# Kernel optimization log

Measured on AMD Instinct MI355X. Metric: run time of the kernel, lower is better.

Reference implementation:

```python
import jax, jax.numpy as jnp
import numpy as np

H = 16
DH = 64
THETA = 10000.0


def setup_inputs() -> dict:
    key = jax.random.key(0)
    ks = jax.random.split(key, 9)
    B, M, R = 4, 1024, 256
    d = H * DH
    s = 0.05
    return {
        "Pq": jax.random.normal(ks[0], (B, M, R), jnp.float32) * s,
        "Pk": jax.random.normal(ks[1], (B, M, R), jnp.float32) * s,
        "Pv": jax.random.normal(ks[2], (B, M, R), jnp.float32) * s,
        "Vq": jax.random.normal(ks[3], (R, d), jnp.float32) * s,
        "Vk": jax.random.normal(ks[4], (R, d), jnp.float32) * s,
        "Vv": jax.random.normal(ks[5], (R, d), jnp.float32) * s,
        "bq": jax.random.normal(ks[6], (d,), jnp.float32) * s,
        "bk": jax.random.normal(ks[7], (d,), jnp.float32) * s,
        "bv": jax.random.normal(ks[8], (d,), jnp.float32) * s,
        "attention_mask": jnp.ones((B, M), jnp.int32),
        "position_ids": jnp.tile(jnp.arange(M, dtype=jnp.int32), (B, 1)),
    }


def _rope_cos_sin(position_ids):
    # half-dim frequencies, matching the kernel's half-half rotation
    half = DH // 2
    inv_freq = 1.0 / (THETA ** (jnp.arange(0, half, dtype=jnp.float32) / half))
    ang = position_ids.astype(jnp.float32)[..., None] * inv_freq  # [B,M,half]
    return jnp.cos(ang), jnp.sin(ang)


def _rotate(x, cos, sin):
    # x: [B,H,M,dh]; cos/sin: [B,M,half] -> broadcast over heads
    half = DH // 2
    x0, x1 = x[..., :half], x[..., half:]
    c = cos[:, None, :, :]
    s = sin[:, None, :, :]
    return jnp.concatenate([x0 * c - x1 * s, x0 * s + x1 * c], axis=-1)


def reference(Pq, Pk, Pv, Vq, Vk, Vv, bq, bk, bv, attention_mask, position_ids):
    B, M, R = Pq.shape
    # reconstruct per-head Q/K/V from low-rank factors
    Vq3 = Vq.reshape(R, H, DH)
    Vk3 = Vk.reshape(R, H, DH)
    Vv3 = Vv.reshape(R, H, DH)
    q = jnp.einsum("bmr,rhd->bhmd", Pq, Vq3) + bq.reshape(H, DH)[None, :, None, :]
    k = jnp.einsum("bmr,rhd->bhmd", Pk, Vk3) + bk.reshape(H, DH)[None, :, None, :]
    v = jnp.einsum("bmr,rhd->bhmd", Pv, Vv3) + bv.reshape(H, DH)[None, :, None, :]
    cos, sin = _rope_cos_sin(position_ids)
    q = _rotate(q, cos, sin)
    k = _rotate(k, cos, sin)
    scale = 1.0 / jnp.sqrt(jnp.float32(DH))
    scores = jnp.einsum("bhmd,bhnd->bhmn", q, k) * scale  # [B,H,M,M]
    valid = attention_mask.astype(bool)
    pad = valid[:, None, :, None] & valid[:, None, None, :]
    scores = jnp.where(pad, scores, -jnp.inf)
    p = jax.nn.softmax(scores, axis=-1)
    out = jnp.einsum("bhmn,bhnd->bhmd", p, v)
    return out
```

## Files before the change

### kernel.cpp

```cpp
#include <hip/hip_runtime.h>
#include <hip/hip_bf16.h>
#include <math.h>

#define BB 4
#define MM 1024
#define RR 256
#define HH 16
#define DHH 64
#define DD (HH*DHH)

typedef __attribute__((ext_vector_type(8))) short short8;
typedef __attribute__((ext_vector_type(4))) float f32x4;

static __device__ __forceinline__ unsigned short f2bf(float x) {
    __hip_bfloat16 h = __float2bfloat16(x);
    return *(unsigned short*)&h;
}

#if defined(__has_builtin)
#  if __has_builtin(__builtin_amdgcn_exp2f)
#    define EXP2F(x) __builtin_amdgcn_exp2f(x)
#  endif
#endif
#ifndef EXP2F
#  define EXP2F(x) __expf((x) * 0.6931471805599453f)
#endif

static __device__ __forceinline__ unsigned pack_bf16_rh(float a, float b) {
    unsigned ua = __builtin_bit_cast(unsigned, a) + 0x8000u;
    unsigned ub = __builtin_bit_cast(unsigned, b) + 0x8000u;
    return __builtin_amdgcn_perm(ub, ua, 0x07060302u);
}

__global__ __launch_bounds__(256) void prep_kernel(
    const float* __restrict__ Pq, const float* __restrict__ Pk, const float* __restrict__ Pv,
    const float* __restrict__ Vq, const float* __restrict__ Vk, const float* __restrict__ Vv,
    __hip_bfloat16* __restrict__ VTq, __hip_bfloat16* __restrict__ VTk,
    __hip_bfloat16* __restrict__ VTv, __hip_bfloat16* __restrict__ Pb)
{
    const int t = threadIdx.x;
    if (blockIdx.x < 768) {
        const int z   = blockIdx.x / 256;
        const int rem = blockIdx.x % 256;
        const int r0  = (rem & 7) * 32;
        const int d0  = (rem >> 3) * 32;
        const float* V = (z == 0) ? Vq : (z == 1) ? Vk : Vv;
        __hip_bfloat16* VT = (z == 0) ? VTq : (z == 1) ? VTk : VTv;

        __shared__ __hip_bfloat16 Ts[32][33];
        {
            const int row = t >> 3;
            const int c4  = (t & 7) * 4;
            float4 f = *(const float4*)&V[(size_t)(r0 + row) * DD + d0 + c4];
            Ts[row][c4 + 0] = __float2bfloat16(f.x);
            Ts[row][c4 + 1] = __float2bfloat16(f.y);
            Ts[row][c4 + 2] = __float2bfloat16(f.z);
            Ts[row][c4 + 3] = __float2bfloat16(f.w);
        }
        __syncthreads();
        {
            const int orow = t >> 3;
            const int oc4  = (t & 7) * 4;
            union { unsigned short u[4]; uint2 v; } pk;
            #pragma unroll
            for (int i = 0; i < 4; ++i) pk.u[i] = *(unsigned short*)&Ts[oc4 + i][orow];
            *(uint2*)&VT[(size_t)(d0 + orow) * RR + r0 + oc4] = pk.v;
        }
    } else {
        const size_t n4 = (size_t)BB * MM * RR / 4;
        size_t i = (size_t)(blockIdx.x - 768) * 256 + t;
        const int which = (int)(i / n4);
        const size_t off = i - (size_t)which * n4;
        const float* P = (which == 0) ? Pq : (which == 1) ? Pk : Pv;
        float4 f = *(const float4*)(P + off * 4);
        union { unsigned short u[4]; uint2 v; } pk;
        pk.u[0] = f2bf(f.x); pk.u[1] = f2bf(f.y); pk.u[2] = f2bf(f.z); pk.u[3] = f2bf(f.w);
        *(uint2*)((unsigned short*)Pb + (size_t)which * BB * MM * RR + off * 4) = pk.v;
    }
}

__global__ __launch_bounds__(256) void svd_gemm(
    const __hip_bfloat16* __restrict__ Pb,
    const __hip_bfloat16* __restrict__ VTq, const __hip_bfloat16* __restrict__ VTk,
    const __hip_bfloat16* __restrict__ VTv,
    const float* __restrict__ bq, const float* __restrict__ bk, const float* __restrict__ bv,
    const int* __restrict__ pos_ids,
    __hip_bfloat16* __restrict__ qout, __hip_bfloat16* __restrict__ kout,
    __hip_bfloat16* __restrict__ vTout)
{
    const int which = blockIdx.z;
    const short* P = (const short*)Pb + (size_t)which * BB * MM * RR;
    const __hip_bfloat16* VT = (which == 0) ? VTq : (which == 1) ? VTk : VTv;
    const float* bias        = (which == 0) ? bq : (which == 1) ? bk : bv;

    const int h   = blockIdx.y;
    const int bm0 = blockIdx.x * 256;
    const int b   = bm0 >> 10;
    const int m0  = bm0 & 1023;
    const int tid = threadIdx.x;
    const int lane = tid & 63;
    const int w    = tid >> 6;
    const int l15  = lane & 15;
    const int quad = lane >> 4;

    __shared__ alignas(16) short SM[256 * 72 + 64 * 72];
    short* As = SM;
    short* Bs = SM + 256 * 72;

    f32x4 acc[4][4];
    #pragma unroll
    for (int mt = 0; mt < 4; ++mt)
        #pragma unroll
        for (int dt = 0; dt < 4; ++dt) acc[mt][dt] = (f32x4){0.f, 0.f, 0.f, 0.f};

    for (int kc = 0; kc < 4; ++kc) {
        #pragma unroll
        for (int i = 0; i < 8; ++i) {
            int u = tid + i * 256;
            int row = u >> 3;
            int cg  = (u & 7) * 8;
            *(uint4*)&As[row * 72 + cg] =
                *(const uint4*)&P[(size_t)(bm0 + row) * RR + kc * 64 + cg];
        }
        #pragma unroll
        for (int i = 0; i < 2; ++i) {
            int u = tid + i * 256;
            int row = u >> 3;
            int cg  = (u & 7) * 8;
            *(uint4*)&Bs[row * 72 + cg] =
                *(const uint4*)((const short*)VT + (size_t)(h * 64 + row) * RR + kc * 64 + cg);
        }
        __syncthreads();

        #pragma unroll
        for (int ks = 0; ks < 2; ++ks) {
            short8 a[4];
            #pragma unroll
            for (int mt = 0; mt < 4; ++mt)
                a[mt] = *(const short8*)&As[(w * 64 + mt * 16 + l15) * 72 + ks * 32 + quad * 8];
            #pragma unroll
            for (int dt = 0; dt < 4; ++dt) {
                short8 bf = *(const short8*)&Bs[(dt * 16 + l15) * 72 + ks * 32 + quad * 8];
                #pragma unroll
                for (int mt = 0; mt < 4; ++mt)
                    acc[mt][dt] = __builtin_amdgcn_mfma_f32_16x16x32_bf16(a[mt], bf, acc[mt][dt], 0, 0, 0);
            }
        }
        __syncthreads();
    }

    #pragma unroll
    for (int dt = 0; dt < 4; ++dt) {
        float bc = bias[h * 64 + dt * 16 + l15];
        #pragma unroll
        for (int mt = 0; mt < 4; ++mt)
            #pragma unroll
            for (int r = 0; r < 4; ++r) acc[mt][dt][r] += bc;
    }

    if (which < 2) {
        __hip_bfloat16* out = (which == 0) ? qout : kout;
        int pm[4][4];
        #pragma unroll
        for (int mt = 0; mt < 4; ++mt)
            #pragma unroll
            for (int r = 0; r < 4; ++r)
                pm[mt][r] = pos_ids[bm0 + w * 64 + mt * 16 + quad * 4 + r];
        float cB[2][4][4], sB[2][4][4];
        #pragma unroll
        for (int f2 = 0; f2 < 2; ++f2) {
            float invf = __powf(10000.0f, -(float)(f2 * 16 + l15) * (1.0f / 32.0f));
            #pragma unroll
            for (int mt = 0; mt < 4; ++mt)
                #pragma unroll
                for (int r = 0; r < 4; ++r) {
                    float ang = (float)pm[mt][r] * invf;
                    __sincosf(ang, &sB[f2][mt][r], &cB[f2][mt][r]);
                }
        }
        #pragma unroll
        for (int dt = 0; dt < 4; ++dt) {
            const int cd = dt * 16 + l15;
            const int f2 = dt & 1;
            #pragma unroll
            for (int mt = 0; mt < 4; ++mt)
                #pragma unroll
                for (int r = 0; r < 4; ++r) {
                    float x  = acc[mt][dt][r];
                    float xp = acc[mt][dt ^ 2][r];
                    float c = cB[f2][mt][r], s = sB[f2][mt][r];
                    float val = (dt < 2) ? (x * c - xp * s) : (xp * s + x * c);
                    int m = m0 + w * 64 + mt * 16 + quad * 4 + r;
                    out[(((size_t)b * HH + h) * MM + m) * DHH + cd] = __float2bfloat16(val);
                }
        }
    } else {
        short* Tt = SM;
        __syncthreads();
        #pragma unroll
        for (int dt = 0; dt < 4; ++dt)
            #pragma unroll
            for (int mt = 0; mt < 4; ++mt) {
                union { unsigned short u[4]; uint2 v; } pk;
                #pragma unroll
                for (int r = 0; r < 4; ++r) pk.u[r] = f2bf(acc[mt][dt][r]);
                *(uint2*)&Tt[(dt * 16 + l15) * 264 + w * 64 + mt * 16 + quad * 4] = pk.v;
            }
        __syncthreads();
        #pragma unroll
        for (int it = 0; it < 8; ++it) {
            int u = tid + it * 256;
            int row = u >> 5;
            int seg = u & 31;
            *(uint4*)&vTout[(((size_t)b * HH + h) * DHH + row) * MM + m0 + seg * 8] =
                *(const uint4*)&Tt[row * 264 + seg * 8];
        }
    }
}

__global__ __launch_bounds__(256, 2) void attn_kernel(
    const __hip_bfloat16* __restrict__ q, const __hip_bfloat16* __restrict__ k,
    const __hip_bfloat16* __restrict__ vT,
    const int* __restrict__ mask, float* __restrict__ out)
{
    const int bh   = blockIdx.x & 63;
    const int qt   = blockIdx.x >> 6;
    const int b    = bh >> 4;
    const int tid  = threadIdx.x;
    const int lane = tid & 63;
    const int w    = tid >> 6;
    const int l15  = lane & 15;
    const int quad = lane >> 4;
    const int q0   = qt * 128;

    __shared__ alignas(16) __hip_bfloat16 Kt[128][72];
    __shared__ alignas(16) __hip_bfloat16 Vt[64][136];

    const short* kbase = (const short*)k  + (size_t)bh * MM * DHH;
    const short* vbase = (const short*)vT + (size_t)bh * DHH * MM;

    short8 qa[2][2];
    #pragma unroll
    for (int mt = 0; mt < 2; ++mt) {
        const short* qb = (const short*)q +
            ((size_t)bh * MM + q0 + w * 32 + mt * 16 + l15) * DHH + quad * 8;
        qa[mt][0] = *(const short8*)(qb);
        qa[mt][1] = *(const short8*)(qb + 32);
    }

    f32x4 Ot[2][4];
    #pragma unroll
    for (int mt = 0; mt < 2; ++mt)
        #pragma unroll
        for (int dt = 0; dt < 4; ++dt) Ot[mt][dt] = (f32x4){0.f, 0.f, 0.f, 0.f};
    float lsum[2] = {0.f, 0.f};

    const int* maskb = mask + b * MM;
    const int srcbase = (lane & 48) | ((lane & 48) >> 2);
    const float k2 = 0.125f * 1.44269504089f;

    for (int nc = 0; nc < MM / 128; ++nc) {
        const int n0 = nc * 128;
        #pragma unroll
        for (int pass = 0; pass < 4; ++pass) {
            int u   = tid + pass * 256;
            int row = u >> 3;
            int cg  = u & 7;
            *(uint4*)&Kt[row][cg * 8] =
                *(const uint4*)(kbase + (size_t)(n0 + row) * DHH + cg * 8);
        }
        #pragma unroll
        for (int pass = 0; pass < 4; ++pass) {
            int u   = tid + pass * 256;
            int row = u >> 4;
            int c   = u & 15;
            union { uint4 q4; uint2 h2[2]; } vld;
            vld.q4 = *(const uint4*)(vbase + (size_t)row * MM + n0 + c * 8);
            int g  = c >> 3;
            int c6 = c & 7;
            int base0 = g * 64 + (c6 >> 2) * 32 + (c6 & 1) * 16 + ((c6 >> 1) & 1) * 4;
            *(uint2*)&Vt[row][base0]     = vld.h2[0];
            *(uint2*)&Vt[row][base0 + 8] = vld.h2[1];
        }
        __syncthreads();

        unsigned long long bal0 = __ballot(maskb[n0 + lane] != 0);
        unsigned long long bal1 = __ballot(maskb[n0 + 64 + lane] != 0);

        f32x4 S[2][8];
        #pragma unroll
        for (int t = 0; t < 8; ++t) {
            const short* kr = (const short*)&Kt[t * 16 + l15][quad * 8];
            short8 ka0 = *(const short8*)(kr);
            short8 ka1 = *(const short8*)(kr + 32);
            #pragma unroll
            for (int mt = 0; mt < 2; ++mt) {
                f32x4 c = (f32x4){0.f, 0.f, 0.f, 0.f};
                c = __builtin_amdgcn_mfma_f32_16x16x32_bf16(ka0, qa[mt][0], c, 0, 0, 0);
                c = __builtin_amdgcn_mfma_f32_16x16x32_bf16(ka1, qa[mt][1], c, 0, 0, 0);
                S[mt][t] = c;
            }
        }

        #pragma unroll
        for (int t = 0; t < 8; ++t) {
            unsigned bits = (unsigned)((t < 4 ? bal0 : bal1) >> ((t & 3) * 16 + quad * 4));
            #pragma unroll
            for (int r = 0; r < 4; ++r) {
                float sb = ((bits >> r) & 1u) ? 0.0f : -1e30f;
                #pragma unroll
                for (int mt = 0; mt < 2; ++mt) {
                    float e = EXP2F(fmaf(S[mt][t][r], k2, sb));
                    lsum[mt] += e;
                    S[mt][t][r] = e;
                }
            }
        }

        short8 pa[2][4];
        #pragma unroll
        for (int mt = 0; mt < 2; ++mt)
            #pragma unroll
            for (int p = 0; p < 4; ++p) {
                union { unsigned u[4]; short8 s; } pk;
                pk.u[0] = pack_bf16_rh(S[mt][2*p][0],   S[mt][2*p][1]);
                pk.u[1] = pack_bf16_rh(S[mt][2*p][2],   S[mt][2*p][3]);
                pk.u[2] = pack_bf16_rh(S[mt][2*p+1][0], S[mt][2*p+1][1]);
                pk.u[3] = pack_bf16_rh(S[mt][2*p+1][2], S[mt][2*p+1][3]);
                pa[mt][p] = pk.s;
            }

        #pragma unroll
        for (int p = 0; p < 4; ++p) {
            #pragma unroll
            for (int dt = 0; dt < 4; ++dt) {
                short8 vb = *(const short8*)&Vt[dt * 16 + l15][p * 32 + quad * 8];
                #pragma unroll
                for (int mt = 0; mt < 2; ++mt)
                    Ot[mt][dt] = __builtin_amdgcn_mfma_f32_16x16x32_bf16(pa[mt][p], vb, Ot[mt][dt], 0, 0, 0);
            }
        }
        __syncthreads();
    }

    #pragma unroll
    for (int mt = 0; mt < 2; ++mt) {
        float s = lsum[mt];
        s += __shfl_xor(s, 16, 64);
        s += __shfl_xor(s, 32, 64);
        float inv = 1.0f / s;
        float* ob = out + ((size_t)bh * MM + q0 + w * 32 + mt * 16) * DHH;
        #pragma unroll
        for (int r = 0; r < 4; ++r) {
            float ir = __shfl(inv, srcbase + r, 64);
            #pragma unroll
            for (int dt = 0; dt < 4; ++dt)
                ob[(quad * 4 + r) * DHH + dt * 16 + l15] = Ot[mt][dt][r] * ir;
        }
    }
}

extern "C" void kernel_launch(void* const* d_in, const int* in_sizes, int n_in,
                              void* d_out, int out_size, void* d_ws, size_t ws_size,
                              hipStream_t stream) {
    const float* Pq = (const float*)d_in[0];
    const float* Pk = (const float*)d_in[1];
    const float* Pv = (const float*)d_in[2];
    const float* Vq = (const float*)d_in[3];
    const float* Vk = (const float*)d_in[4];
    const float* Vv = (const float*)d_in[5];
    const float* bq = (const float*)d_in[6];
    const float* bk = (const float*)d_in[7];
    const float* bv = (const float*)d_in[8];
    const int* mask = (const int*)d_in[9];
    const int* pos  = (const int*)d_in[10];
    float* out = (float*)d_out;

    const size_t qkv_elems = (size_t)BB * HH * MM * DHH;
    __hip_bfloat16* qb  = (__hip_bfloat16*)d_ws;
    __hip_bfloat16* kb  = qb + qkv_elems;
    __hip_bfloat16* vT  = kb + qkv_elems;
    __hip_bfloat16* VTq = vT + qkv_elems;
    __hip_bfloat16* VTk = VTq + (size_t)DD * RR;
    __hip_bfloat16* VTv = VTk + (size_t)DD * RR;
    __hip_bfloat16* Pb  = VTv + (size_t)DD * RR;

    prep_kernel<<<768 + 3 * BB * MM * RR / 4 / 256, 256, 0, stream>>>(
        Pq, Pk, Pv, Vq, Vk, Vv, VTq, VTk, VTv, Pb);

    dim3 gG(BB * MM / 256, HH, 3);
    svd_gemm<<<gG, 256, 0, stream>>>(Pb, VTq, VTk, VTv, bq, bk, bv, pos, qb, kb, vT);

    attn_kernel<<<BB * HH * (MM / 128), 256, 0, stream>>>(qb, kb, vT, mask, out);
}
```

Before: 135.3 us.

## Fuse P fp32-to-bf16 conversion into GEMM and retile to 64 rows by 4 heads

The prep kernel no longer converts Pq/Pk/Pv to bf16 in a separate pass. The GEMM now reads fp32 P directly and packs it to bf16 while staging into shared memory. The GEMM tile changes from 256 rows by 1 head to 64 rows by 4 heads, so each P tile is reused across four heads. The V-transpose epilogue is reorganised into two passes through a smaller shared buffer. This removes a full write and reread of a bf16 copy of P. In exchange, each block reads fp32 P (twice the bytes per element) and the grid shape changes, which shifts per-block MFMA work and occupancy.

```diff
diff --git a/kernel.cpp b/kernel.cpp
--- a/kernel.cpp
+++ b/kernel.cpp
@@ -33,54 +33,41 @@
 }
 
 __global__ __launch_bounds__(256) void prep_kernel(
-    const float* __restrict__ Pq, const float* __restrict__ Pk, const float* __restrict__ Pv,
     const float* __restrict__ Vq, const float* __restrict__ Vk, const float* __restrict__ Vv,
     __hip_bfloat16* __restrict__ VTq, __hip_bfloat16* __restrict__ VTk,
-    __hip_bfloat16* __restrict__ VTv, __hip_bfloat16* __restrict__ Pb)
+    __hip_bfloat16* __restrict__ VTv)
 {
-    const int t = threadIdx.x;
-    if (blockIdx.x < 768) {
-        const int z   = blockIdx.x / 256;
-        const int rem = blockIdx.x % 256;
-        const int r0  = (rem & 7) * 32;
-        const int d0  = (rem >> 3) * 32;
-        const float* V = (z == 0) ? Vq : (z == 1) ? Vk : Vv;
-        __hip_bfloat16* VT = (z == 0) ? VTq : (z == 1) ? VTk : VTv;
-
-        __shared__ __hip_bfloat16 Ts[32][33];
-        {
-            const int row = t >> 3;
-            const int c4  = (t & 7) * 4;
-            float4 f = *(const float4*)&V[(size_t)(r0 + row) * DD + d0 + c4];
-            Ts[row][c4 + 0] = __float2bfloat16(f.x);
-            Ts[row][c4 + 1] = __float2bfloat16(f.y);
-            Ts[row][c4 + 2] = __float2bfloat16(f.z);
-            Ts[row][c4 + 3] = __float2bfloat16(f.w);
-        }
-        __syncthreads();
-        {
-            const int orow = t >> 3;
-            const int oc4  = (t & 7) * 4;
-            union { unsigned short u[4]; uint2 v; } pk;
-            #pragma unroll
-            for (int i = 0; i < 4; ++i) pk.u[i] = *(unsigned short*)&Ts[oc4 + i][orow];
-            *(uint2*)&VT[(size_t)(d0 + orow) * RR + r0 + oc4] = pk.v;
-        }
-    } else {
-        const size_t n4 = (size_t)BB * MM * RR / 4;
-        size_t i = (size_t)(blockIdx.x - 768) * 256 + t;
-        const int which = (int)(i / n4);
-        const size_t off = i - (size_t)which * n4;
-        const float* P = (which == 0) ? Pq : (which == 1) ? Pk : Pv;
-        float4 f = *(const float4*)(P + off * 4);
+    const int t   = threadIdx.x;
+    const int z   = blockIdx.x / 256;
+    const int rem = blockIdx.x % 256;
+    const int r0  = (rem & 7) * 32;
+    const int d0  = (rem >> 3) * 32;
+    const float* V = (z == 0) ? Vq : (z == 1) ? Vk : Vv;
+    __hip_bfloat16* VT = (z == 0) ? VTq : (z == 1) ? VTk : VTv;
+
+    __shared__ __hip_bfloat16 Ts[32][33];
+    {
+        const int row = t >> 3;
+        const int c4  = (t & 7) * 4;
+        float4 f = *(const float4*)&V[(size_t)(r0 + row) * DD + d0 + c4];
+        Ts[row][c4 + 0] = __float2bfloat16(f.x);
+        Ts[row][c4 + 1] = __float2bfloat16(f.y);
+        Ts[row][c4 + 2] = __float2bfloat16(f.z);
+        Ts[row][c4 + 3] = __float2bfloat16(f.w);
+    }
+    __syncthreads();
+    {
+        const int orow = t >> 3;
+        const int oc4  = (t & 7) * 4;
         union { unsigned short u[4]; uint2 v; } pk;
-        pk.u[0] = f2bf(f.x); pk.u[1] = f2bf(f.y); pk.u[2] = f2bf(f.z); pk.u[3] = f2bf(f.w);
-        *(uint2*)((unsigned short*)Pb + (size_t)which * BB * MM * RR + off * 4) = pk.v;
+        #pragma unroll
+        for (int i = 0; i < 4; ++i) pk.u[i] = *(unsigned short*)&Ts[oc4 + i][orow];
+        *(uint2*)&VT[(size_t)(d0 + orow) * RR + r0 + oc4] = pk.v;
     }
 }
 
 __global__ __launch_bounds__(256) void svd_gemm(
-    const __hip_bfloat16* __restrict__ Pb,
+    const float* __restrict__ Pq, const float* __restrict__ Pk, const float* __restrict__ Pv,
     const __hip_bfloat16* __restrict__ VTq, const __hip_bfloat16* __restrict__ VTk,
     const __hip_bfloat16* __restrict__ VTv,
     const float* __restrict__ bq, const float* __restrict__ bk, const float* __restrict__ bv,
@@ -89,12 +76,12 @@
     __hip_bfloat16* __restrict__ vTout)
 {
     const int which = blockIdx.z;
-    const short* P = (const short*)Pb + (size_t)which * BB * MM * RR;
+    const float* P           = (which == 0) ? Pq : (which == 1) ? Pk : Pv;
     const __hip_bfloat16* VT = (which == 0) ? VTq : (which == 1) ? VTk : VTv;
     const float* bias        = (which == 0) ? bq : (which == 1) ? bk : bv;
 
-    const int h   = blockIdx.y;
-    const int bm0 = blockIdx.x * 256;
+    const int hg  = blockIdx.y;
+    const int bm0 = blockIdx.x * 64;
     const int b   = bm0 >> 10;
     const int m0  = bm0 & 1023;
     const int tid = threadIdx.x;
@@ -103,117 +90,111 @@
     const int l15  = lane & 15;
     const int quad = lane >> 4;
 
-    __shared__ alignas(16) short SM[256 * 72 + 64 * 72];
+    __shared__ alignas(16) short SM[(64 + 256) * 72];
     short* As = SM;
-    short* Bs = SM + 256 * 72;
-
-    f32x4 acc[4][4];
-    #pragma unroll
-    for (int mt = 0; mt < 4; ++mt)
-        #pragma unroll
-        for (int dt = 0; dt < 4; ++dt) acc[mt][dt] = (f32x4){0.f, 0.f, 0.f, 0.f};
+    short* Bs = SM + 64 * 72;
+
+    f32x4 acc[16];
+    #pragma unroll
+    for (int dt = 0; dt < 16; ++dt) acc[dt] = (f32x4){0.f, 0.f, 0.f, 0.f};
 
     for (int kc = 0; kc < 4; ++kc) {
         #pragma unroll
+        for (int i = 0; i < 4; ++i) {
+            int u   = tid + i * 256;
+            int row = u >> 4;
+            int c4  = (u & 15) * 4;
+            float4 f = *(const float4*)&P[(size_t)(bm0 + row) * RR + kc * 64 + c4];
+            uint2 pk;
+            pk.x = pack_bf16_rh(f.x, f.y);
+            pk.y = pack_bf16_rh(f.z, f.w);
+            *(uint2*)&As[row * 72 + c4] = pk;
+        }
+        #pragma unroll
         for (int i = 0; i < 8; ++i) {
-            int u = tid + i * 256;
-            int row = u >> 3;
-            int cg  = (u & 7) * 8;
-            *(uint4*)&As[row * 72 + cg] =
-                *(const uint4*)&P[(size_t)(bm0 + row) * RR + kc * 64 + cg];
-        }
-        #pragma unroll
-        for (int i = 0; i < 2; ++i) {
-            int u = tid + i * 256;
+            int u   = tid + i * 256;
             int row = u >> 3;
             int cg  = (u & 7) * 8;
             *(uint4*)&Bs[row * 72 + cg] =
-                *(const uint4*)((const short*)VT + (size_t)(h * 64 + row) * RR + kc * 64 + cg);
+                *(const uint4*)((const short*)VT + (size_t)(hg * 256 + row) * RR + kc * 64 + cg);
         }
         __syncthreads();
 
         #pragma unroll
         for (int ks = 0; ks < 2; ++ks) {
-            short8 a[4];
-            #pragma unroll
-            for (int mt = 0; mt < 4; ++mt)
-                a[mt] = *(const short8*)&As[(w * 64 + mt * 16 + l15) * 72 + ks * 32 + quad * 8];
-            #pragma unroll
-            for (int dt = 0; dt < 4; ++dt) {
+            short8 a = *(const short8*)&As[(w * 16 + l15) * 72 + ks * 32 + quad * 8];
+            #pragma unroll
+            for (int dt = 0; dt < 16; ++dt) {
                 short8 bf = *(const short8*)&Bs[(dt * 16 + l15) * 72 + ks * 32 + quad * 8];
-                #pragma unroll
-                for (int mt = 0; mt < 4; ++mt)
-                    acc[mt][dt] = __builtin_amdgcn_mfma_f32_16x16x32_bf16(a[mt], bf, acc[mt][dt], 0, 0, 0);
+                acc[dt] = __builtin_amdgcn_mfma_f32_16x16x32_bf16(a, bf, acc[dt], 0, 0, 0);
             }
         }
         __syncthreads();
     }
 
     #pragma unroll
-    for (int dt = 0; dt < 4; ++dt) {
-        float bc = bias[h * 64 + dt * 16 + l15];
-        #pragma unroll
-        for (int mt = 0; mt < 4; ++mt)
-            #pragma unroll
-            for (int r = 0; r < 4; ++r) acc[mt][dt][r] += bc;
+    for (int dt = 0; dt < 16; ++dt) {
+        float bc = bias[hg * 256 + dt * 16 + l15];
+        #pragma unroll
+        for (int r = 0; r < 4; ++r) acc[dt][r] += bc;
     }
 
     if (which < 2) {
         __hip_bfloat16* out = (which == 0) ? qout : kout;
-        int pm[4][4];
-        #pragma unroll
-        for (int mt = 0; mt < 4; ++mt)
-            #pragma unroll
-            for (int r = 0; r < 4; ++r)
-                pm[mt][r] = pos_ids[bm0 + w * 64 + mt * 16 + quad * 4 + r];
-        float cB[2][4][4], sB[2][4][4];
+        int pm[4];
+        #pragma unroll
+        for (int r = 0; r < 4; ++r)
+            pm[r] = pos_ids[bm0 + w * 16 + quad * 4 + r];
+        float cB[2][4], sB[2][4];
         #pragma unroll
         for (int f2 = 0; f2 < 2; ++f2) {
             float invf = __powf(10000.0f, -(float)(f2 * 16 + l15) * (1.0f / 32.0f));
             #pragma unroll
-            for (int mt = 0; mt < 4; ++mt)
-                #pragma unroll
-                for (int r = 0; r < 4; ++r) {
-                    float ang = (float)pm[mt][r] * invf;
-                    __sincosf(ang, &sB[f2][mt][r], &cB[f2][mt][r]);
-                }
-        }
-        #pragma unroll
-        for (int dt = 0; dt < 4; ++dt) {
-            const int cd = dt * 16 + l15;
+            for (int r = 0; r < 4; ++r) {
+                float ang = (float)pm[r] * invf;
+                __sincosf(ang, &sB[f2][r], &cB[f2][r]);
+            }
+        }
+        #pragma unroll
+        for (int dt = 0; dt < 16; ++dt) {
+            const int h  = hg * 4 + (dt >> 2);
+            const int cd = (dt & 3) * 16 + l15;
             const int f2 = dt & 1;
             #pragma unroll
-            for (int mt = 0; mt < 4; ++mt)
-                #pragma unroll
-                for (int r = 0; r < 4; ++r) {
-                    float x  = acc[mt][dt][r];
-                    float xp = acc[mt][dt ^ 2][r];
-                    float c = cB[f2][mt][r], s = sB[f2][mt][r];
-                    float val = (dt < 2) ? (x * c - xp * s) : (xp * s + x * c);
-                    int m = m0 + w * 64 + mt * 16 + quad * 4 + r;
-                    out[(((size_t)b * HH + h) * MM + m) * DHH + cd] = __float2bfloat16(val);
-                }
+            for (int r = 0; r < 4; ++r) {
+                float x  = acc[dt][r];
+                float xp = acc[dt ^ 2][r];
+                float c = cB[f2][r], s = sB[f2][r];
+                float val = ((dt & 3) < 2) ? (x * c - xp * s) : (xp * s + x * c);
+                int m = m0 + w * 16 + quad * 4 + r;
+                out[(((size_t)b * HH + h) * MM + m) * DHH + cd] = __float2bfloat16(val);
+            }
         }
     } else {
         short* Tt = SM;
-        __syncthreads();
-        #pragma unroll
-        for (int dt = 0; dt < 4; ++dt)
-            #pragma unroll
-            for (int mt = 0; mt < 4; ++mt) {
-                union { unsigned short u[4]; uint2 v; } pk;
-                #pragma unroll
-                for (int r = 0; r < 4; ++r) pk.u[r] = f2bf(acc[mt][dt][r]);
-                *(uint2*)&Tt[(dt * 16 + l15) * 264 + w * 64 + mt * 16 + quad * 4] = pk.v;
-            }
-        __syncthreads();
-        #pragma unroll
-        for (int it = 0; it < 8; ++it) {
-            int u = tid + it * 256;
-            int row = u >> 5;
-            int seg = u & 31;
-            *(uint4*)&vTout[(((size_t)b * HH + h) * DHH + row) * MM + m0 + seg * 8] =
-                *(const uint4*)&Tt[row * 264 + seg * 8];
+        #pragma unroll
+        for (int pp = 0; pp < 2; ++pp) {
+            __syncthreads();
+            #pragma unroll
+            for (int dt2 = 0; dt2 < 8; ++dt2) {
+                int dt = pp * 8 + dt2;
+                uint2 pk;
+                pk.x = pack_bf16_rh(acc[dt][0], acc[dt][1]);
+                pk.y = pack_bf16_rh(acc[dt][2], acc[dt][3]);
+                *(uint2*)&Tt[(dt2 * 16 + l15) * 72 + w * 16 + quad * 4] = pk;
+            }
+            __syncthreads();
+            #pragma unroll
+            for (int i = 0; i < 4; ++i) {
+                int u   = tid + i * 256;
+                int row = u >> 3;
+                int seg = u & 7;
+                int dl  = pp * 128 + row;
+                int h   = hg * 4 + (dl >> 6);
+                int din = dl & 63;
+                *(uint4*)&vTout[(((size_t)b * HH + h) * DHH + din) * MM + m0 + seg * 8] =
+                    *(const uint4*)&Tt[row * 72 + seg * 8];
+            }
         }
     }
 }
@@ -383,13 +364,12 @@
     __hip_bfloat16* VTq = vT + qkv_elems;
     __hip_bfloat16* VTk = VTq + (size_t)DD * RR;
     __hip_bfloat16* VTv = VTk + (size_t)DD * RR;
-    __hip_bfloat16* Pb  = VTv + (size_t)DD * RR;
-
-    prep_kernel<<<768 + 3 * BB * MM * RR / 4 / 256, 256, 0, stream>>>(
-        Pq, Pk, Pv, Vq, Vk, Vv, VTq, VTk, VTv, Pb);
-
-    dim3 gG(BB * MM / 256, HH, 3);
-    svd_gemm<<<gG, 256, 0, stream>>>(Pb, VTq, VTk, VTv, bq, bk, bv, pos, qb, kb, vT);
+
+    prep_kernel<<<768, 256, 0, stream>>>(Vq, Vk, Vv, VTq, VTk, VTv);
+
+    dim3 gG(BB * MM / 64, HH / 4, 3);
+    svd_gemm<<<gG, 256, 0, stream>>>(Pq, Pk, Pv, VTq, VTk, VTv, bq, bk, bv, pos,
+                                     qb, kb, vT);
 
     attn_kernel<<<BB * HH * (MM / 128), 256, 0, stream>>>(qb, kb, vT, mask, out);
 }
```

New measurement: 156.4 us. 15.6% more time.
